# Kernel tuning notes

Measured on AMD Instinct MI355X. Metric: run time of the kernel, lower is better.

## Reference

```python
import jax, jax.numpy as jnp
import numpy as np

BN_EPS = 1e-5


def setup_inputs() -> dict:
    key = jax.random.key(0)
    ks = jax.random.split(key, 6)
    B, N, M, C1, C2 = 8, 8192, 2048, 128, 256
    in_ch = C1 + C2  # 384
    return {
        "xyz1": jax.random.uniform(ks[0], (B, N, 3), dtype=jnp.float32),
        "xyz2": jax.random.uniform(ks[1], (B, M, 3), dtype=jnp.float32),
        "features1": jax.random.normal(ks[2], (B, C1, N), dtype=jnp.float32),
        "features2": jax.random.normal(ks[3], (B, C2, M), dtype=jnp.float32),
        # Conv1d(kernel_size=1, bias=False) weights, squeezed to [out, in]
        "conv_w0": jax.random.normal(ks[4], (256, in_ch), dtype=jnp.float32) * 0.05,
        "gamma0": jnp.ones((256,), dtype=jnp.float32),
        "beta0": jnp.zeros((256,), dtype=jnp.float32),
        "conv_w1": jax.random.normal(ks[5], (256, 256), dtype=jnp.float32) * 0.05,
        "gamma1": jnp.ones((256,), dtype=jnp.float32),
        "beta1": jnp.zeros((256,), dtype=jnp.float32),
    }


def _conv_bn_relu(x, w, gamma, beta):
    # 1x1 Conv1d (no bias) == per-point channel matmul: [B,Cin,N] -> [B,Cout,N]
    x = jnp.einsum("oc,bcn->bon", w, x)
    # BatchNorm1d in training mode: batch stats over (B, N), biased variance
    mu = jnp.mean(x, axis=(0, 2), keepdims=True)
    var = jnp.var(x, axis=(0, 2), keepdims=True)
    x = (x - mu) * jax.lax.rsqrt(var + BN_EPS)
    x = x * gamma[None, :, None] + beta[None, :, None]
    return jax.nn.relu(x)


def reference(xyz1, xyz2, features1, features2,
              conv_w0, gamma0, beta0, conv_w1, gamma1, beta1):
    # squared pairwise distances [B, N, M] (broadcast diff reduced over coord dim)
    diff = xyz1[:, :, None, :] - xyz2[:, None, :, :]  # [B,N,M,3]
    dists = jnp.sum(diff * diff, axis=-1)             # [B,N,M]
    idx = jnp.argmin(dists, axis=-1)                  # [B,N] nearest downsampled point

    # per-batch gather: features2[b, :, idx[b]] -> [B, C2, N]
    interp = jax.vmap(lambda f, i: f[:, i])(features2, idx)

    x = jnp.concatenate([features1, interp], axis=1)  # [B, C1+C2, N]
    x = _conv_bn_relu(x, conv_w0, gamma0, beta0)
    x = _conv_bn_relu(x, conv_w1, gamma1, beta1)
    return x
```

## Files before the change

### kernel.cpp

```cpp
#include <hip/hip_runtime.h>
#include <stdint.h>

typedef unsigned short u16;
typedef unsigned int u32;
typedef __attribute__((ext_vector_type(8))) short short8;
typedef __attribute__((ext_vector_type(4))) float floatx4;

__device__ __forceinline__ u16 f2b(float f) {
  union { float f; u32 u; } c; c.f = f;
  u32 u = c.u;
  u += 0x7fffu + ((u >> 16) & 1u);
  return (u16)(u >> 16);
}
__device__ __forceinline__ float b2f(u16 h) {
  union { u32 u; float f; } c; c.u = ((u32)h) << 16;
  return c.f;
}

__device__ __forceinline__ void glds16(const void* g, void* l) {
  __builtin_amdgcn_global_load_lds((__attribute__((address_space(1))) void*)g,
                                   (__attribute__((address_space(3))) void*)l, 16, 0, 0);
}

__global__ void prep_k(const float* __restrict__ w0, const float* __restrict__ w1,
                       u16* __restrict__ w0b, u16* __restrict__ w1b, float* __restrict__ sums) {
  int blk = blockIdx.x, t = threadIdx.x;
  int i = blk * 256 + t;
  if (blk < 384) w0b[i] = f2b(w0[i]);
  else { int j = i - 98304; w1b[j] = f2b(w1[j]); }
  if (blk < 4) sums[i] = 0.f;
}

__global__ void transpose_cast_k(const float* __restrict__ in, u16* __restrict__ out, int C, int N) {
  __shared__ u16 tile[64][72];
  int b = blockIdx.z;
  int c0 = blockIdx.y * 64, n0 = blockIdx.x * 64;
  const float* src = in + ((size_t)b * C + c0) * N + n0;
  int t = threadIdx.x;
#pragma unroll
  for (int i = 0; i < 4; i++) {
    int id = t + i * 256;
    int c = id >> 4, nq = (id & 15) * 4;
    float4 v = *(const float4*)(src + (size_t)c * N + nq);
    tile[nq + 0][c] = f2b(v.x);
    tile[nq + 1][c] = f2b(v.y);
    tile[nq + 2][c] = f2b(v.z);
    tile[nq + 3][c] = f2b(v.w);
  }
  __syncthreads();
  int n = t >> 2, ch = (t & 3) * 16;
  u16* dst = out + ((size_t)b * N + n0 + n) * C + c0 + ch;
  uint4 a = *(const uint4*)&tile[n][ch];
  uint4 bb = *(const uint4*)&tile[n][ch + 8];
  *(uint4*)dst = a;
  *(uint4*)(dst + 8) = bb;
}

__global__ void argmin_part_k(const float* __restrict__ xyz1, const float* __restrict__ xyz2,
                              float2* __restrict__ cand) {
  __shared__ float4 s2[256];
  int b = blockIdx.z, mq = blockIdx.y, nq = blockIdx.x;
  const float* x2 = xyz2 + ((size_t)b * 2048 + mq * 256) * 3;
  int t = threadIdx.x;
  s2[t] = make_float4(x2[t * 3], x2[t * 3 + 1], x2[t * 3 + 2], 0.f);
  __syncthreads();
  int n0 = nq * 1024 + t;
  float px[4], py[4], pz[4];
#pragma unroll
  for (int q = 0; q < 4; q++) {
    const float* p1 = xyz1 + ((size_t)b * 8192 + n0 + q * 256) * 3;
    px[q] = p1[0]; py[q] = p1[1]; pz[q] = p1[2];
  }
  float best[4] = {3.0e38f, 3.0e38f, 3.0e38f, 3.0e38f};
  int bi[4] = {0, 0, 0, 0};
#pragma unroll 4
  for (int m = 0; m < 256; m++) {
    float4 qq = s2[m];
#pragma unroll
    for (int q = 0; q < 4; q++) {
      float dx = px[q] - qq.x, dy = py[q] - qq.y, dz = pz[q] - qq.z;
      float d = fmaf(dz, dz, fmaf(dy, dy, dx * dx));
      bool c = d < best[q];
      best[q] = c ? d : best[q];
      bi[q] = c ? m : bi[q];
    }
  }
#pragma unroll
  for (int q = 0; q < 4; q++) {
    int n = n0 + q * 256;
    cand[(size_t)mq * 65536 + (size_t)b * 8192 + n] =
        make_float2(best[q], __int_as_float(mq * 256 + bi[q]));
  }
}

__global__ __launch_bounds__(512) void gemm1_k(const u16* __restrict__ w0b, const u16* __restrict__ f1t,
                                               const u16* __restrict__ f2t, const float2* __restrict__ cand,
                                               u16* __restrict__ y0) {
  __shared__ u16 As[256 * 64];
  __shared__ u16 Bs[128 * 64];
  __shared__ int sidx[128];
  int t = threadIdx.x;
  int pt0 = blockIdx.x * 128;
  int b = pt0 >> 13;
  if (t < 128) {
    int p = pt0 + t;
    float bd = 3.0e38f; int bi = 0;
#pragma unroll
    for (int qc = 0; qc < 8; qc++) {
      float2 c = cand[(size_t)qc * 65536 + p];
      if (c.x < bd) { bd = c.x; bi = __float_as_int(c.y); }
    }
    sidx[t] = bi;
  }
  floatx4 zero = {0.f, 0.f, 0.f, 0.f};
  floatx4 acc[4][4];
#pragma unroll
  for (int i = 0; i < 4; i++)
#pragma unroll
    for (int j = 0; j < 4; j++) acc[i][j] = zero;
  int lane = t & 63, wave = t >> 6;
  int wrow = (wave >> 1) * 64, wcol = (wave & 1) * 64;
  int lr = lane & 15, lq = lane >> 4;
  int srow = lane >> 3;
  int sch = ((lane & 7) ^ srow) * 8;
  __syncthreads();
  int prow[2], gidx[2];
#pragma unroll
  for (int i = 0; i < 2; i++) {
    prow[i] = (wave * 2 + i) * 8 + srow;
    gidx[i] = sidx[prow[i]];
  }

#pragma unroll
  for (int k0 = 0; k0 < 384; k0 += 64) {
    __syncthreads();
#pragma unroll
    for (int i = 0; i < 4; i++) {
      int chunkA = wave * 4 + i;
      glds16(w0b + (size_t)(chunkA * 8 + srow) * 384 + k0 + sch, &As[chunkA * 512]);
    }
    if (k0 < 128) {
#pragma unroll
      for (int i = 0; i < 2; i++)
        glds16(f1t + (size_t)(pt0 + prow[i]) * 128 + k0 + sch, &Bs[(wave * 2 + i) * 512]);
    } else {
#pragma unroll
      for (int i = 0; i < 2; i++)
        glds16(f2t + ((size_t)(b << 11) + gidx[i]) * 256 + (k0 - 128) + sch, &Bs[(wave * 2 + i) * 512]);
    }
    __syncthreads();
#pragma unroll
    for (int ks = 0; ks < 2; ks++) {
      short8 af[4], bf[4];
#pragma unroll
      for (int i = 0; i < 4; i++) {
        int row = wrow + i * 16 + lr;
        af[i] = *(const short8*)&As[row * 64 + ((((ks << 2) | lq) ^ (lr & 7)) << 3)];
      }
#pragma unroll
      for (int j = 0; j < 4; j++) {
        int row = wcol + j * 16 + lr;
        bf[j] = *(const short8*)&Bs[row * 64 + ((((ks << 2) | lq) ^ (lr & 7)) << 3)];
      }
#pragma unroll
      for (int i = 0; i < 4; i++)
#pragma unroll
        for (int j = 0; j < 4; j++)
          acc[i][j] = __builtin_amdgcn_mfma_f32_16x16x32_bf16(af[i], bf[j], acc[i][j], 0, 0, 0);
    }
  }
#pragma unroll
  for (int i = 0; i < 4; i++) {
#pragma unroll
    for (int j = 0; j < 4; j++) {
      int o = wrow + i * 16 + lq * 4;
      int p = pt0 + wcol + j * 16 + lr;
      uint2 pk;
      pk.x = (u32)f2b(acc[i][j][0]) | ((u32)f2b(acc[i][j][1]) << 16);
      pk.y = (u32)f2b(acc[i][j][2]) | ((u32)f2b(acc[i][j][3]) << 16);
      *(uint2*)&y0[(size_t)p * 256 + o] = pk;
    }
  }
}

__global__ __launch_bounds__(512) void gemm2_k(const u16* __restrict__ w1b, const u16* __restrict__ y0,
                                               const float* __restrict__ sum0, const float* __restrict__ sq0,
                                               const float* __restrict__ gamma0, const float* __restrict__ beta0,
                                               u16* __restrict__ y1) {
  __shared__ u16 As[256 * 64];
  __shared__ u16 Bs[128 * 72];
  __shared__ float ssc[256], ssh[256];
  int t = threadIdx.x;
  if (t < 256) {
    float mean = sum0[t] * (1.f / 65536.f);
    float var = fmaxf(sq0[t] * (1.f / 65536.f) - mean * mean, 0.f);
    float r = rsqrtf(var + 1e-5f);
    float sc = gamma0[t] * r;
    ssc[t] = sc;
    ssh[t] = beta0[t] - mean * sc;
  }
  int pt0 = blockIdx.x * 128;
  floatx4 zero = {0.f, 0.f, 0.f, 0.f};
  floatx4 acc[4][4];
#pragma unroll
  for (int i = 0; i < 4; i++)
#pragma unroll
    for (int j = 0; j < 4; j++) acc[i][j] = zero;
  int lane = t & 63, wave = t >> 6;
  int wrow = (wave >> 1) * 64, wcol = (wave & 1) * 64;
  int lr = lane & 15, lq = lane >> 4;
  int srow = lane >> 3;
  int sch = ((lane & 7) ^ srow) * 8;

#pragma unroll
  for (int k0 = 0; k0 < 256; k0 += 64) {
    __syncthreads();
#pragma unroll
    for (int i = 0; i < 4; i++) {
      int chunkA = wave * 4 + i;
      glds16(w1b + (size_t)(chunkA * 8 + srow) * 256 + k0 + sch, &As[chunkA * 512]);
    }
#pragma unroll
    for (int i = 0; i < 2; i++) {
      int id = t + i * 512;
      int row = id >> 3, ch = (id & 7) * 8;
      uint4 raw = *(const uint4*)(y0 + (size_t)(pt0 + row) * 256 + k0 + ch);
      u32 rw[4] = {raw.x, raw.y, raw.z, raw.w};
      u32 ow[4];
#pragma unroll
      for (int w = 0; w < 4; w++) {
        int k = k0 + ch + w * 2;
        float v0 = b2f((u16)(rw[w] & 0xffffu));
        float v1 = b2f((u16)(rw[w] >> 16));
        v0 = fmaxf(v0 * ssc[k] + ssh[k], 0.f);
        v1 = fmaxf(v1 * ssc[k + 1] + ssh[k + 1], 0.f);
        ow[w] = (u32)f2b(v0) | ((u32)f2b(v1) << 16);
      }
      uint4 ov; ov.x = ow[0]; ov.y = ow[1]; ov.z = ow[2]; ov.w = ow[3];
      *(uint4*)&Bs[row * 72 + ch] = ov;
    }
    __syncthreads();
#pragma unroll
    for (int ks = 0; ks < 2; ks++) {
      int kk = ks * 32 + lq * 8;
      short8 af[4], bf[4];
#pragma unroll
      for (int i = 0; i < 4; i++) {
        int row = wrow + i * 16 + lr;
        af[i] = *(const short8*)&As[row * 64 + ((((ks << 2) | lq) ^ (lr & 7)) << 3)];
      }
#pragma unroll
      for (int j = 0; j < 4; j++) bf[j] = *(const short8*)&Bs[(wcol + j * 16 + lr) * 72 + kk];
#pragma unroll
      for (int i = 0; i < 4; i++)
#pragma unroll
        for (int j = 0; j < 4; j++)
          acc[i][j] = __builtin_amdgcn_mfma_f32_16x16x32_bf16(af[i], bf[j], acc[i][j], 0, 0, 0);
    }
  }
#pragma unroll
  for (int i = 0; i < 4; i++) {
#pragma unroll
    for (int j = 0; j < 4; j++) {
      int o = wrow + i * 16 + lq * 4;
      int p = pt0 + wcol + j * 16 + lr;
      uint2 pk;
      pk.x = (u32)f2b(acc[i][j][0]) | ((u32)f2b(acc[i][j][1]) << 16);
      pk.y = (u32)f2b(acc[i][j][2]) | ((u32)f2b(acc[i][j][3]) << 16);
      *(uint2*)&y1[(size_t)p * 256 + o] = pk;
    }
  }
}

__global__ void stats_k(const u16* __restrict__ y, float* __restrict__ sum, float* __restrict__ sq) {
  __shared__ float ls[8][256];
  __shared__ float lqd[8][256];
  int t = threadIdx.x;
  int c8 = (t & 31) * 8;
  int p0 = t >> 5;
  float s[8] = {0.f, 0.f, 0.f, 0.f, 0.f, 0.f, 0.f, 0.f};
  float q[8] = {0.f, 0.f, 0.f, 0.f, 0.f, 0.f, 0.f, 0.f};
  const u16* base = y + (size_t)blockIdx.x * 65536;
  for (int it = 0; it < 32; it++) {
    int p = p0 + it * 8;
    uint4 raw = *(const uint4*)(base + (size_t)p * 256 + c8);
    u32 rw[4] = {raw.x, raw.y, raw.z, raw.w};
#pragma unroll
    for (int w = 0; w < 4; w++) {
      float v0 = b2f((u16)(rw[w] & 0xffffu));
      float v1 = b2f((u16)(rw[w] >> 16));
      s[w * 2] += v0;     q[w * 2] += v0 * v0;
      s[w * 2 + 1] += v1; q[w * 2 + 1] += v1 * v1;
    }
  }
#pragma unroll
  for (int e = 0; e < 8; e++) { ls[p0][c8 + e] = s[e]; lqd[p0][c8 + e] = q[e]; }
  __syncthreads();
  if (t < 256) {
    float ss = 0.f, qq = 0.f;
#pragma unroll
    for (int r = 0; r < 8; r++) { ss += ls[r][t]; qq += lqd[r][t]; }
    atomicAdd(&sum[t], ss);
    atomicAdd(&sq[t], qq);
  }
}

__global__ void finalize_k(const u16* __restrict__ y1, const float* __restrict__ sum1,
                           const float* __restrict__ sq1, const float* __restrict__ gamma1,
                           const float* __restrict__ beta1, float* __restrict__ out) {
  __shared__ float tile[64][65];
  __shared__ float fs[64], fh[64];
  int b = blockIdx.z, o0 = blockIdx.y * 64, n0 = blockIdx.x * 64;
  int t = threadIdx.x;
  if (t < 64) {
    int o = o0 + t;
    float mean = sum1[o] * (1.f / 65536.f);
    float var = fmaxf(sq1[o] * (1.f / 65536.f) - mean * mean, 0.f);
    float r = rsqrtf(var + 1e-5f);
    float sc = gamma1[o] * r;
    fs[t] = sc;
    fh[t] = beta1[o] - mean * sc;
  }
  __syncthreads();
  int pl = t >> 2, ch = (t & 3) * 16;
  const u16* src = y1 + ((size_t)(b * 8192 + n0 + pl)) * 256 + o0 + ch;
  uint4 r0 = *(const uint4*)src;
  uint4 r1 = *(const uint4*)(src + 8);
  u16 hv[16];
  *(uint4*)&hv[0] = r0;
  *(uint4*)&hv[8] = r1;
#pragma unroll
  for (int e = 0; e < 16; e++) {
    float v = b2f(hv[e]) * fs[ch + e] + fh[ch + e];
    tile[pl][ch + e] = fmaxf(v, 0.f);
  }
  __syncthreads();
  int ol = t >> 2, nch = (t & 3) * 16;
  float* dst = out + ((size_t)(b * 256 + o0 + ol)) * 8192 + n0 + nch;
#pragma unroll
  for (int j = 0; j < 16; j += 4) {
    float4 v = make_float4(tile[nch + j][ol], tile[nch + j + 1][ol],
                           tile[nch + j + 2][ol], tile[nch + j + 3][ol]);
    *(float4*)(dst + j) = v;
  }
}

extern "C" void kernel_launch(void* const* d_in, const int* in_sizes, int n_in,
                              void* d_out, int out_size, void* d_ws, size_t ws_size,
                              hipStream_t stream) {
  const float* xyz1      = (const float*)d_in[0];
  const float* xyz2      = (const float*)d_in[1];
  const float* features1 = (const float*)d_in[2];
  const float* features2 = (const float*)d_in[3];
  const float* conv_w0   = (const float*)d_in[4];
  const float* gamma0    = (const float*)d_in[5];
  const float* beta0     = (const float*)d_in[6];
  const float* conv_w1   = (const float*)d_in[7];
  const float* gamma1    = (const float*)d_in[8];
  const float* beta1     = (const float*)d_in[9];
  float* out = (float*)d_out;

  char* ws = (char*)d_ws;
  size_t off = 0;
  auto alloc = [&](size_t bytes) {
    char* p = ws + off;
    off = (off + bytes + 4095) & ~(size_t)4095;
    return p;
  };
  float*  sums = (float*)alloc(4 * 256 * 4);
  u16*    w0b  = (u16*)alloc(256 * 384 * 2);
  u16*    w1b  = (u16*)alloc(256 * 256 * 2);
  float2* cand = (float2*)alloc((size_t)8 * 65536 * 8);
  u16*    f1t  = (u16*)alloc((size_t)65536 * 128 * 2);
  u16*    f2t  = (u16*)alloc((size_t)16384 * 256 * 2);
  u16*    y0   = (u16*)alloc((size_t)65536 * 256 * 2);
  u16*    y1   = (u16*)alloc((size_t)65536 * 256 * 2);

  prep_k<<<dim3(640), 256, 0, stream>>>(conv_w0, conv_w1, w0b, w1b, sums);
  argmin_part_k<<<dim3(8, 8, 8), 256, 0, stream>>>(xyz1, xyz2, cand);
  transpose_cast_k<<<dim3(128, 2, 8), 256, 0, stream>>>(features1, f1t, 128, 8192);
  transpose_cast_k<<<dim3(32, 4, 8), 256, 0, stream>>>(features2, f2t, 256, 2048);
  gemm1_k<<<dim3(512), 512, 0, stream>>>(w0b, f1t, f2t, cand, y0);
  stats_k<<<dim3(256), 256, 0, stream>>>(y0, sums + 0, sums + 256);
  gemm2_k<<<dim3(512), 512, 0, stream>>>(w1b, y0, sums + 0, sums + 256, gamma0, beta0, y1);
  stats_k<<<dim3(256), 256, 0, stream>>>(y1, sums + 512, sums + 768);
  finalize_k<<<dim3(128, 4, 8), 256, 0, stream>>>(y1, sums + 512, sums + 768, gamma1, beta1, out);
}
```

Measured before the change: 249.9 us.

## Merge prep kernels into one launch and fuse BN statistics into GEMM epilogues

The four preprocessing kernels (weight cast, argmin partials, two transpose-casts) become one kernel that dispatches on block index. The two separate stats passes, which re-read y0 and y1, are removed. Per-channel sum and sum-of-squares are now computed in each GEMM epilogue from the fp32 accumulators, using shuffles, LDS atomics and global atomics. This saves launches and two full reads of the 32MB intermediates. Stats now come from fp32 rather than bf16-rounded values, and the extra epilogue syncs and atomics add some cost.

```diff
diff --git a/kernel.cpp b/kernel.cpp
--- a/kernel.cpp
+++ b/kernel.cpp
@@ -22,79 +22,82 @@
                                    (__attribute__((address_space(3))) void*)l, 16, 0, 0);
 }
 
-__global__ void prep_k(const float* __restrict__ w0, const float* __restrict__ w1,
-                       u16* __restrict__ w0b, u16* __restrict__ w1b, float* __restrict__ sums) {
+__global__ void prep_all_k(const float* __restrict__ xyz1, const float* __restrict__ xyz2,
+                           float2* __restrict__ cand,
+                           const float* __restrict__ f1, u16* __restrict__ f1t,
+                           const float* __restrict__ f2, u16* __restrict__ f2t,
+                           const float* __restrict__ w0, u16* __restrict__ w0b,
+                           const float* __restrict__ w1, u16* __restrict__ w1b,
+                           float* __restrict__ sums) {
+  __shared__ __align__(16) char smem[9216];
   int blk = blockIdx.x, t = threadIdx.x;
-  int i = blk * 256 + t;
-  if (blk < 384) w0b[i] = f2b(w0[i]);
-  else { int j = i - 98304; w1b[j] = f2b(w1[j]); }
-  if (blk < 4) sums[i] = 0.f;
-}
-
-__global__ void transpose_cast_k(const float* __restrict__ in, u16* __restrict__ out, int C, int N) {
-  __shared__ u16 tile[64][72];
-  int b = blockIdx.z;
-  int c0 = blockIdx.y * 64, n0 = blockIdx.x * 64;
-  const float* src = in + ((size_t)b * C + c0) * N + n0;
-  int t = threadIdx.x;
-#pragma unroll
-  for (int i = 0; i < 4; i++) {
-    int id = t + i * 256;
-    int c = id >> 4, nq = (id & 15) * 4;
-    float4 v = *(const float4*)(src + (size_t)c * N + nq);
-    tile[nq + 0][c] = f2b(v.x);
-    tile[nq + 1][c] = f2b(v.y);
-    tile[nq + 2][c] = f2b(v.z);
-    tile[nq + 3][c] = f2b(v.w);
-  }
-  __syncthreads();
-  int n = t >> 2, ch = (t & 3) * 16;
-  u16* dst = out + ((size_t)b * N + n0 + n) * C + c0 + ch;
-  uint4 a = *(const uint4*)&tile[n][ch];
-  uint4 bb = *(const uint4*)&tile[n][ch + 8];
-  *(uint4*)dst = a;
-  *(uint4*)(dst + 8) = bb;
-}
-
-__global__ void argmin_part_k(const float* __restrict__ xyz1, const float* __restrict__ xyz2,
-                              float2* __restrict__ cand) {
-  __shared__ float4 s2[256];
-  int b = blockIdx.z, mq = blockIdx.y, nq = blockIdx.x;
-  const float* x2 = xyz2 + ((size_t)b * 2048 + mq * 256) * 3;
-  int t = threadIdx.x;
-  s2[t] = make_float4(x2[t * 3], x2[t * 3 + 1], x2[t * 3 + 2], 0.f);
-  __syncthreads();
-  int n0 = nq * 1024 + t;
-  float px[4], py[4], pz[4];
-#pragma unroll
-  for (int q = 0; q < 4; q++) {
-    const float* p1 = xyz1 + ((size_t)b * 8192 + n0 + q * 256) * 3;
-    px[q] = p1[0]; py[q] = p1[1]; pz[q] = p1[2];
-  }
-  float best[4] = {3.0e38f, 3.0e38f, 3.0e38f, 3.0e38f};
-  int bi[4] = {0, 0, 0, 0};
+  if (blk < 512) {
+    float4* s2 = (float4*)smem;
+    int nq = blk & 7, mq = (blk >> 3) & 7, b = blk >> 6;
+    const float* x2 = xyz2 + ((size_t)b * 2048 + mq * 256) * 3;
+    s2[t] = make_float4(x2[t * 3], x2[t * 3 + 1], x2[t * 3 + 2], 0.f);
+    __syncthreads();
+    int n0 = nq * 1024 + t;
+    float px[4], py[4], pz[4];
+#pragma unroll
+    for (int q = 0; q < 4; q++) {
+      const float* p1 = xyz1 + ((size_t)b * 8192 + n0 + q * 256) * 3;
+      px[q] = p1[0]; py[q] = p1[1]; pz[q] = p1[2];
+    }
+    float best[4] = {3.0e38f, 3.0e38f, 3.0e38f, 3.0e38f};
+    int bi[4] = {0, 0, 0, 0};
 #pragma unroll 4
-  for (int m = 0; m < 256; m++) {
-    float4 qq = s2[m];
+    for (int m = 0; m < 256; m++) {
+      float4 qq = s2[m];
+#pragma unroll
+      for (int q = 0; q < 4; q++) {
+        float dx = px[q] - qq.x, dy = py[q] - qq.y, dz = pz[q] - qq.z;
+        float d = fmaf(dz, dz, fmaf(dy, dy, dx * dx));
+        bool c = d < best[q];
+        best[q] = c ? d : best[q];
+        bi[q] = c ? m : bi[q];
+      }
+    }
 #pragma unroll
     for (int q = 0; q < 4; q++) {
-      float dx = px[q] - qq.x, dy = py[q] - qq.y, dz = pz[q] - qq.z;
-      float d = fmaf(dz, dz, fmaf(dy, dy, dx * dx));
-      bool c = d < best[q];
-      best[q] = c ? d : best[q];
-      bi[q] = c ? m : bi[q];
-    }
-  }
-#pragma unroll
-  for (int q = 0; q < 4; q++) {
-    int n = n0 + q * 256;
-    cand[(size_t)mq * 65536 + (size_t)b * 8192 + n] =
-        make_float2(best[q], __int_as_float(mq * 256 + bi[q]));
+      int n = n0 + q * 256;
+      cand[(size_t)mq * 65536 + (size_t)b * 8192 + n] =
+          make_float2(best[q], __int_as_float(mq * 256 + bi[q]));
+    }
+  } else if (blk < 3584) {
+    const float* in; u16* out; int C, N, bx, by, bz;
+    if (blk < 2560) { int rel = blk - 512;  in = f1; out = f1t; C = 128; N = 8192; bx = rel & 127; by = (rel >> 7) & 1; bz = rel >> 8; }
+    else            { int rel = blk - 2560; in = f2; out = f2t; C = 256; N = 2048; bx = rel & 31;  by = (rel >> 5) & 3; bz = rel >> 7; }
+    u16 (*tile)[72] = (u16(*)[72])smem;
+    int c0 = by * 64, n0 = bx * 64;
+    const float* src = in + ((size_t)bz * C + c0) * N + n0;
+#pragma unroll
+    for (int i = 0; i < 4; i++) {
+      int id = t + i * 256;
+      int c = id >> 4, nq = (id & 15) * 4;
+      float4 v = *(const float4*)(src + (size_t)c * N + nq);
+      tile[nq + 0][c] = f2b(v.x);
+      tile[nq + 1][c] = f2b(v.y);
+      tile[nq + 2][c] = f2b(v.z);
+      tile[nq + 3][c] = f2b(v.w);
+    }
+    __syncthreads();
+    int n = t >> 2, ch = (t & 3) * 16;
+    u16* dst = out + ((size_t)bz * N + n0 + n) * C + c0 + ch;
+    *(uint4*)dst = *(const uint4*)&tile[n][ch];
+    *(uint4*)(dst + 8) = *(const uint4*)&tile[n][ch + 8];
+  } else {
+    int rel = blk - 3584;
+    int i = rel * 256 + t;
+    if (rel < 384) w0b[i] = f2b(w0[i]);
+    else { int j = i - 98304; w1b[j] = f2b(w1[j]); }
+    if (rel < 4) sums[i] = 0.f;
   }
 }
 
 __global__ __launch_bounds__(512) void gemm1_k(const u16* __restrict__ w0b, const u16* __restrict__ f1t,
                                                const u16* __restrict__ f2t, const float2* __restrict__ cand,
+                                               float* __restrict__ sum0, float* __restrict__ sq0,
                                                u16* __restrict__ y0) {
   __shared__ u16 As[256 * 64];
   __shared__ u16 Bs[128 * 64];
@@ -181,11 +184,37 @@
       *(uint2*)&y0[(size_t)p * 256 + o] = pk;
     }
   }
+  __syncthreads();
+  float* red = (float*)As;
+  red[t] = 0.f;
+  __syncthreads();
+#pragma unroll
+  for (int i = 0; i < 4; i++) {
+#pragma unroll
+    for (int r = 0; r < 4; r++) {
+      float s = acc[i][0][r] + acc[i][1][r] + acc[i][2][r] + acc[i][3][r];
+      float q = acc[i][0][r] * acc[i][0][r] + acc[i][1][r] * acc[i][1][r] +
+                acc[i][2][r] * acc[i][2][r] + acc[i][3][r] * acc[i][3][r];
+#pragma unroll
+      for (int m = 8; m >= 1; m >>= 1) { s += __shfl_xor(s, m); q += __shfl_xor(q, m); }
+      if (lr == 0) {
+        int o = wrow + i * 16 + lq * 4 + r;
+        atomicAdd(&red[o], s);
+        atomicAdd(&red[256 + o], q);
+      }
+    }
+  }
+  __syncthreads();
+  if (t < 256) {
+    atomicAdd(&sum0[t], red[t]);
+    atomicAdd(&sq0[t], red[256 + t]);
+  }
 }
 
 __global__ __launch_bounds__(512) void gemm2_k(const u16* __restrict__ w1b, const u16* __restrict__ y0,
                                                const float* __restrict__ sum0, const float* __restrict__ sq0,
                                                const float* __restrict__ gamma0, const float* __restrict__ beta0,
+                                               float* __restrict__ sum1, float* __restrict__ sq1,
                                                u16* __restrict__ y1) {
   __shared__ u16 As[256 * 64];
   __shared__ u16 Bs[128 * 72];
@@ -270,38 +299,30 @@
       *(uint2*)&y1[(size_t)p * 256 + o] = pk;
     }
   }
-}
-
-__global__ void stats_k(const u16* __restrict__ y, float* __restrict__ sum, float* __restrict__ sq) {
-  __shared__ float ls[8][256];
-  __shared__ float lqd[8][256];
-  int t = threadIdx.x;
-  int c8 = (t & 31) * 8;
-  int p0 = t >> 5;
-  float s[8] = {0.f, 0.f, 0.f, 0.f, 0.f, 0.f, 0.f, 0.f};
-  float q[8] = {0.f, 0.f, 0.f, 0.f, 0.f, 0.f, 0.f, 0.f};
-  const u16* base = y + (size_t)blockIdx.x * 65536;
-  for (int it = 0; it < 32; it++) {
-    int p = p0 + it * 8;
-    uint4 raw = *(const uint4*)(base + (size_t)p * 256 + c8);
-    u32 rw[4] = {raw.x, raw.y, raw.z, raw.w};
-#pragma unroll
-    for (int w = 0; w < 4; w++) {
-      float v0 = b2f((u16)(rw[w] & 0xffffu));
-      float v1 = b2f((u16)(rw[w] >> 16));
-      s[w * 2] += v0;     q[w * 2] += v0 * v0;
-      s[w * 2 + 1] += v1; q[w * 2 + 1] += v1 * v1;
-    }
-  }
-#pragma unroll
-  for (int e = 0; e < 8; e++) { ls[p0][c8 + e] = s[e]; lqd[p0][c8 + e] = q[e]; }
+  __syncthreads();
+  float* red = (float*)As;
+  red[t] = 0.f;
+  __syncthreads();
+#pragma unroll
+  for (int i = 0; i < 4; i++) {
+#pragma unroll
+    for (int r = 0; r < 4; r++) {
+      float s = acc[i][0][r] + acc[i][1][r] + acc[i][2][r] + acc[i][3][r];
+      float q = acc[i][0][r] * acc[i][0][r] + acc[i][1][r] * acc[i][1][r] +
+                acc[i][2][r] * acc[i][2][r] + acc[i][3][r] * acc[i][3][r];
+#pragma unroll
+      for (int m = 8; m >= 1; m >>= 1) { s += __shfl_xor(s, m); q += __shfl_xor(q, m); }
+      if (lr == 0) {
+        int o = wrow + i * 16 + lq * 4 + r;
+        atomicAdd(&red[o], s);
+        atomicAdd(&red[256 + o], q);
+      }
+    }
+  }
   __syncthreads();
   if (t < 256) {
-    float ss = 0.f, qq = 0.f;
-#pragma unroll
-    for (int r = 0; r < 8; r++) { ss += ls[r][t]; qq += lqd[r][t]; }
-    atomicAdd(&sum[t], ss);
-    atomicAdd(&sq[t], qq);
+    atomicAdd(&sum1[t], red[t]);
+    atomicAdd(&sq1[t], red[256 + t]);
   }
 }
 
@@ -376,13 +397,10 @@
   u16*    y0   = (u16*)alloc((size_t)65536 * 256 * 2);
   u16*    y1   = (u16*)alloc((size_t)65536 * 256 * 2);
 
-  prep_k<<<dim3(640), 256, 0, stream>>>(conv_w0, conv_w1, w0b, w1b, sums);
-  argmin_part_k<<<dim3(8, 8, 8), 256, 0, stream>>>(xyz1, xyz2, cand);
-  transpose_cast_k<<<dim3(128, 2, 8), 256, 0, stream>>>(features1, f1t, 128, 8192);
-  transpose_cast_k<<<dim3(32, 4, 8), 256, 0, stream>>>(features2, f2t, 256, 2048);
-  gemm1_k<<<dim3(512), 512, 0, stream>>>(w0b, f1t, f2t, cand, y0);
-  stats_k<<<dim3(256), 256, 0, stream>>>(y0, sums + 0, sums + 256);
-  gemm2_k<<<dim3(512), 512, 0, stream>>>(w1b, y0, sums + 0, sums + 256, gamma0, beta0, y1);
-  stats_k<<<dim3(256), 256, 0, stream>>>(y1, sums + 512, sums + 768);
+  prep_all_k<<<dim3(4224), 256, 0, stream>>>(xyz1, xyz2, cand, features1, f1t,
+                                             features2, f2t, conv_w0, w0b, conv_w1, w1b, sums);
+  gemm1_k<<<dim3(512), 512, 0, stream>>>(w0b, f1t, f2t, cand, sums + 0, sums + 256, y0);
+  gemm2_k<<<dim3(512), 512, 0, stream>>>(w1b, y0, sums + 0, sums + 256, gamma0, beta0,
+                                         sums + 512, sums + 768, y1);
   finalize_k<<<dim3(128, 4, 8), 256, 0, stream>>>(y1, sums + 512, sums + 768, gamma1, beta1, out);
 }
```

New measurement: 243.3 us. -2.6%, faster.
